# Performance work log

Measured on AMD Instinct MI355X. Metric: run time of the kernel, lower is better.

## Reference

```python
import jax, jax.numpy as jnp
import numpy as np

RES = (512, 512)
MAX_VAL = 100.0
OBJ_WIDTH = 5
N_ITERS = 5
SIGMA = 0.2


def setup_inputs() -> dict:
    key = jax.random.key(0)
    ks = jax.random.split(key, 6)
    H, W = RES
    x = jax.random.uniform(ks[0], (1, H, W, 2), jnp.float32) * 2.0 - 1.0  # query grid in [-1,1]
    boundary_types = jax.random.randint(ks[1], (H, W), 0, 2, jnp.int32)
    boundary_conditions = jax.random.uniform(ks[2], (H, W), jnp.float32)
    B_enc = SIGMA * jax.random.normal(ks[3], (64, 2), jnp.float32)  # GaussianEncoding(0.2, 2, 64)
    Wh = jax.random.normal(ks[4], (4, 128, 128), jnp.float32) / jnp.sqrt(128.0)
    W_out = jax.random.normal(ks[5], (128, 1), jnp.float32) / jnp.sqrt(128.0)
    return {"x": x, "boundary_types": boundary_types,
            "boundary_conditions": boundary_conditions,
            "B_enc": B_enc, "Wh": Wh, "W_out": W_out}


def _box_filter(a, width):
    # width x width mean filter, 'same' padding (F.conv2d with ones/width^2 kernel)
    k = jnp.ones((1, 1, width, width), a.dtype) / float(width * width)
    return jax.lax.conv_general_dilated(a[None, None], k, (1, 1), "SAME")[0, 0]


def _grid_sample_2d(img, grid):
    # img [H,W]; grid [N,2] with (x,y) in [-1,1]; bilinear, align_corners=True, border padding
    H, W = img.shape
    ix = jnp.clip((grid[:, 0] + 1.0) * 0.5 * (W - 1), 0.0, W - 1.0)
    iy = jnp.clip((grid[:, 1] + 1.0) * 0.5 * (H - 1), 0.0, H - 1.0)
    x0 = jnp.floor(ix).astype(jnp.int32)
    y0 = jnp.floor(iy).astype(jnp.int32)
    x1 = jnp.clip(x0 + 1, 0, W - 1)
    y1 = jnp.clip(y0 + 1, 0, H - 1)
    wx = ix - x0
    wy = iy - y0
    return (img[y0, x0] * (1 - wx) * (1 - wy) + img[y0, x1] * wx * (1 - wy)
            + img[y1, x0] * (1 - wx) * wy + img[y1, x1] * wx * wy)


def _solve(V0, C, boundary_types, boundary_conditions):
    # 5 Jacobi-style 8-neighbor stencil passes: free cells take the neighbor
    # average plus local cost; boundary cells are pinned to their conditions.
    free = boundary_types == 0

    def step(V, _):
        Vp = jnp.pad(V, 1, mode="edge")
        nb = (Vp[:-2, :-2] + Vp[:-2, 1:-1] + Vp[:-2, 2:]
              + Vp[1:-1, :-2] + Vp[1:-1, 2:]
              + Vp[2:, :-2] + Vp[2:, 1:-1] + Vp[2:, 2:]) / 8.0
        return jnp.where(free, nb + C, boundary_conditions), None

    V, _ = jax.lax.scan(step, V0, None, length=N_ITERS)
    return V


def reference(x, boundary_types, boundary_conditions, B_enc, Wh, W_out):
    H, W = RES
    free = boundary_types == 0
    # V init: max_val everywhere, boundary cells pinned (obj_inds = boundary_types > 0)
    V0 = jnp.where(free, jnp.float32(MAX_VAL), boundary_conditions)

    # Gaussian random Fourier feature encoding of 0.5 + 0.5*x -> 128 dims
    xq = 0.5 + 0.5 * x.reshape(-1, 2)
    vp = (2.0 * jnp.pi) * (xq @ B_enc.T)            # [N, 64]
    enc = jnp.concatenate([jnp.cos(vp), jnp.sin(vp)], axis=-1)  # [N, 128]

    # FullyFusedMLP: 4 hidden ReLU layers of 128 neurons, linear 1-dim output, no bias
    h = enc
    for i in range(Wh.shape[0]):
        h = jax.nn.relu(h @ Wh[i])
    C = (h @ W_out).reshape(H, W)
    C_pos = jax.nn.relu(C)

    # extra cost: box-filtered obstacle boundary values splashed onto free cells
    obj = boundary_conditions * (boundary_types == 1) * (boundary_conditions > 0)
    extra = _box_filter(obj, OBJ_WIDTH) * free
    Cs = C_pos + extra

    out_grid = _solve(V0, Cs, boundary_types, boundary_conditions)
    out = _grid_sample_2d(out_grid, x.reshape(-1, 2)).reshape(H, W)
    return out, C
```

## Files before the change

### kernel.cpp

```cpp
#include <hip/hip_runtime.h>
#include <hip/hip_bf16.h>


typedef unsigned short ushort_t;
typedef short short8 __attribute__((ext_vector_type(8)));
typedef float floatx16 __attribute__((ext_vector_type(16)));
typedef unsigned int uintx4 __attribute__((ext_vector_type(4)));

#define HH 512
#define WW 512
#define NPIX (HH*WW)

__device__ inline unsigned int pk_bf16(float a, float b) {
    __hip_bfloat162 h = __float22bfloat162_rn(float2{a, b});
    return *(unsigned int*)&h;
}
__device__ inline void async_copy16(void* lds, const void* g) {
    __builtin_amdgcn_global_load_lds(
        (const __attribute__((address_space(1))) unsigned int*)g,
        (__attribute__((address_space(3))) unsigned int*)lds, 16, 0, 0);
}

__global__ __launch_bounds__(256) void prep_kernel(const float* __restrict__ Wh,
                                                   ushort_t* __restrict__ WT) {
    __shared__ float trans[32][129];
    const int t = threadIdx.x;
    const int l = blockIdx.x >> 2, n0 = (blockIdx.x & 3) * 32;
    const int nl = t & 31, k0 = t >> 5;
    #pragma unroll
    for (int pass = 0; pass < 16; ++pass) {
        int k = pass * 8 + k0;
        trans[nl][k] = Wh[l * 16384 + k * 128 + n0 + nl];
    }
    __syncthreads();
    #pragma unroll
    for (int c = 0; c < 2; ++c) {
        int idx = c * 256 + t;
        int nl2 = idx >> 4, P = idx & 15;
        int n = n0 + nl2;
        int cc = P ^ (n & 15);
        int ks = cc >> 1, Hq = cc & 1;
        int base = (ks >> 1) * 32 + (ks & 1) * 16 + Hq * 4;
        unsigned int w0 = pk_bf16(trans[nl2][base + 0],  trans[nl2][base + 1]);
        unsigned int w1 = pk_bf16(trans[nl2][base + 2],  trans[nl2][base + 3]);
        unsigned int w2 = pk_bf16(trans[nl2][base + 8],  trans[nl2][base + 9]);
        unsigned int w3 = pk_bf16(trans[nl2][base + 10], trans[nl2][base + 11]);
        ((uint4*)WT)[(l * 128 + n) * 16 + P] = uint4{w0, w1, w2, w3};
    }
}

template<int BUF>
__device__ __forceinline__ void klayer(const ushort_t* __restrict__ wlds,
                                       const int (&inn)[8],
                                       const uintx4 (&fragv)[8],
                                       floatx16 (&acc)[4]) {
    #pragma unroll
    for (int i = 0; i < 4; ++i) acc[i] = (floatx16)(0.0f);
    #pragma unroll
    for (int ks = 0; ks < 8; ++ks) {
        short8 bf = __builtin_bit_cast(short8, fragv[ks]);
        #pragma unroll
        for (int i = 0; i < 4; ++i) {
            short8 av = *(const short8*)((const char*)wlds + BUF * 32768 + i * 8192 + inn[ks]);
            acc[i] = __builtin_amdgcn_mfma_f32_32x32x16_bf16(av, bf, acc[i], 0, 0, 0);
        }
    }
}

__device__ __forceinline__ void xform_all(uintx4 (&fragv)[8], const floatx16 (&acc)[4]) {
    #pragma unroll
    for (int ks = 0; ks < 8; ++ks) {
        const int i = ks >> 1, par = ks & 1;
        fragv[ks][0] = pk_bf16(fmaxf(acc[i][8 * par + 0], 0.0f),
                               fmaxf(acc[i][8 * par + 1], 0.0f));
        fragv[ks][1] = pk_bf16(fmaxf(acc[i][8 * par + 2], 0.0f),
                               fmaxf(acc[i][8 * par + 3], 0.0f));
        fragv[ks][2] = pk_bf16(fmaxf(acc[i][8 * par + 4], 0.0f),
                               fmaxf(acc[i][8 * par + 5], 0.0f));
        fragv[ks][3] = pk_bf16(fmaxf(acc[i][8 * par + 6], 0.0f),
                               fmaxf(acc[i][8 * par + 7], 0.0f));
    }
}

__device__ __forceinline__ void stage_layer(ushort_t* wlds, int buf,
                                            const char* src, int wave, int lane) {
    #pragma unroll
    for (int c2 = 0; c2 < 4; ++c2) {
        int base = c2 * 512 + wave * 64;
        async_copy16(&wlds[buf * 16384 + base * 8], src + (base + lane) * 16);
    }
}

__global__ __launch_bounds__(512, 2) void mlp_kernel(const float* __restrict__ x,
                                                     const ushort_t* __restrict__ WT,
                                                     const float* __restrict__ benc,
                                                     const float* __restrict__ wout,
                                                     float* __restrict__ C_ws,
                                                     float* __restrict__ outbuf) {
    __shared__ __align__(16) ushort_t wlds[2 * 128 * 128];
    const int tid = threadIdx.x;
    const int lane = tid & 63, wave = tid >> 6;
    const int m = lane & 31, Hh = lane >> 5;
    const int p0 = blockIdx.x * 256 + wave * 32;

    stage_layer(wlds, 0, (const char*)WT, wave, lane);
    stage_layer(wlds, 1, (const char*)WT + 32768, wave, lane);

    int inn[8];
    #pragma unroll
    for (int ks = 0; ks < 8; ++ks)
        inn[ks] = m * 256 + ((((2 * ks + Hh) ^ (m & 15))) << 4);

    uintx4 fragv[8];

    {
        float2 xv = ((const float2*)x)[p0 + m];
        float xq0 = 0.5f + 0.5f * xv.x, xq1 = 0.5f + 0.5f * xv.y;
        #pragma unroll
        for (int ks = 0; ks < 8; ++ks) {
            const int i = ks >> 1, par = ks & 1;
            #pragma unroll
            for (int jp = 0; jp < 4; ++jp) {
                int nu = i * 32 + par * 16 + Hh * 4 + (jp & 1) * 2 + (jp >> 1) * 8;
                int f = nu & 63;
                float4 b = *(const float4*)&benc[2 * f];
                float t0 = __builtin_amdgcn_fractf(xq0 * b.x + xq1 * b.y);
                float t1 = __builtin_amdgcn_fractf(xq0 * b.z + xq1 * b.w);
                float v0, v1;
                if (ks < 4) { v0 = __builtin_amdgcn_cosf(t0); v1 = __builtin_amdgcn_cosf(t1); }
                else        { v0 = __builtin_amdgcn_sinf(t0); v1 = __builtin_amdgcn_sinf(t1); }
                fragv[ks][jp] = pk_bf16(v0, v1);
            }
        }
    }
    __syncthreads();

    floatx16 acc[4];
    klayer<0>(wlds, inn, fragv, acc);
    __syncthreads();
    stage_layer(wlds, 0, (const char*)WT + 2 * 32768, wave, lane);
    xform_all(fragv, acc);
    klayer<1>(wlds, inn, fragv, acc);
    __syncthreads();
    stage_layer(wlds, 1, (const char*)WT + 3 * 32768, wave, lane);
    xform_all(fragv, acc);
    klayer<0>(wlds, inn, fragv, acc);
    __syncthreads();
    xform_all(fragv, acc);
    klayer<1>(wlds, inn, fragv, acc);

    float s = 0.0f;
    #pragma unroll
    for (int i = 0; i < 4; ++i) {
        #pragma unroll
        for (int rq = 0; rq < 4; ++rq) {
            float4 wv = *(const float4*)&wout[i * 32 + rq * 8 + 4 * Hh];
            s += fmaxf(acc[i][rq * 4 + 0], 0.0f) * wv.x
               + fmaxf(acc[i][rq * 4 + 1], 0.0f) * wv.y
               + fmaxf(acc[i][rq * 4 + 2], 0.0f) * wv.z
               + fmaxf(acc[i][rq * 4 + 3], 0.0f) * wv.w;
        }
    }
    s += __shfl_xor(s, 32);
    if (Hh == 0) {
        C_ws[p0 + m] = s;
        outbuf[NPIX + p0 + m] = s;
    }
}

__global__ __launch_bounds__(256) void fused_solve_kernel(const int* __restrict__ bt,
                                                          const float* __restrict__ bc,
                                                          const float* __restrict__ C_ws,
                                                          float* __restrict__ Vfin) {
    __shared__ float Va[30 * 32];
    __shared__ float Vb[30 * 32];
    __shared__ float Wp[30 * 32];
    const int tid = threadIdx.x;
    const int gx0 = (blockIdx.x & 31) * 16 - 7, gy0 = (blockIdx.x >> 5) * 16 - 7;

    for (int c = tid; c < 30 * 32; c += 256) {
        int li = c >> 5, lj = c & 31;
        int gi = gy0 + li, gj = gx0 + lj;
        float v = 0.0f;
        if (lj < 30 && gi >= 0 && gi < HH && gj >= 0 && gj < WW) {
            int g = gi * WW + gj;
            float b = bc[g];
            if (bt[g] == 1 && b > 0.0f) v = b;
        }
        Va[c] = v;
    }
    __syncthreads();

    for (int c = tid; c < 30 * 32; c += 256) {
        int li = c >> 5, lj = c & 31;
        int gi = gy0 + li, gj = gx0 + lj;
        float w = -1.0f, v0 = 0.0f;
        if (li >= 2 && li < 28 && lj >= 2 && lj < 28 &&
            gi >= 0 && gi < HH && gj >= 0 && gj < WW) {
            int g = gi * WW + gj;
            if (bt[g] == 0) {
                float s = 0.0f;
                #pragma unroll
                for (int di = 0; di < 5; ++di)
                    #pragma unroll
                    for (int dj = 0; dj < 5; ++dj)
                        s += Va[(li + di - 2) * 32 + lj + dj - 2];
                w = fmaxf(C_ws[g], 0.0f) + s * 0.04f;
                v0 = 100.0f;
            } else {
                float b = bc[g];
                w = -b - 1.0f;
                v0 = b;
            }
        }
        Wp[c] = w;
        Vb[c] = v0;
    }
    __syncthreads();

    float* src = Vb;
    float* dst = Va;
    #pragma unroll 1
    for (int t = 0; t < 5; ++t) {
        for (int c = tid; c < 26 * 32; c += 256) {
            int li = 2 + (c >> 5), lj = c & 31;
            if (lj < 2 || lj >= 28) continue;
            float w = Wp[li * 32 + lj];
            float v;
            if (w < 0.0f) {
                v = -w - 1.0f;
            } else {
                int gi = gy0 + li, gj = gx0 + lj;
                int um = (gi > 0)      ? li - 1 : li;
                int dp = (gi < HH - 1) ? li + 1 : li;
                int lm = (gj > 0)      ? lj - 1 : lj;
                int rp = (gj < WW - 1) ? lj + 1 : lj;
                float s = src[um * 32 + lm] + src[um * 32 + lj] + src[um * 32 + rp]
                        + src[li * 32 + lm]                     + src[li * 32 + rp]
                        + src[dp * 32 + lm] + src[dp * 32 + lj] + src[dp * 32 + rp];
                v = s * 0.125f + w;
            }
            dst[li * 32 + lj] = v;
        }
        __syncthreads();
        float* tmp = src; src = dst; dst = tmp;
    }

    {
        int li = 7 + (tid >> 4), lj = 7 + (tid & 15);
        Vfin[(gy0 + li) * WW + gx0 + lj] = src[li * 32 + lj];
    }
}

__global__ void sample_kernel(const float* __restrict__ x,
                              const float* __restrict__ V,
                              float* __restrict__ out) {
    int idx = blockIdx.x * 256 + threadIdx.x;
    float2 g2 = ((const float2*)x)[idx];
    float ix = (g2.x + 1.0f) * 0.5f * 511.0f;
    float iy = (g2.y + 1.0f) * 0.5f * 511.0f;
    ix = fminf(fmaxf(ix, 0.0f), 511.0f);
    iy = fminf(fmaxf(iy, 0.0f), 511.0f);
    int x0 = (int)floorf(ix), y0 = (int)floorf(iy);
    int x1 = min(x0 + 1, 511), y1 = min(y0 + 1, 511);
    float wx = ix - (float)x0, wy = iy - (float)y0;
    float v00 = V[y0 * 512 + x0], v01 = V[y0 * 512 + x1];
    float v10 = V[y1 * 512 + x0], v11 = V[y1 * 512 + x1];
    float v = v00 * (1.0f - wx) * (1.0f - wy) + v01 * wx * (1.0f - wy)
            + v10 * (1.0f - wx) * wy          + v11 * wx * wy;
    out[idx] = v;
}

extern "C" void kernel_launch(void* const* d_in, const int* in_sizes, int n_in,
                              void* d_out, int out_size, void* d_ws, size_t ws_size,
                              hipStream_t stream) {
    const float* x    = (const float*)d_in[0];
    const int*   bt   = (const int*)d_in[1];
    const float* bc   = (const float*)d_in[2];
    const float* benc = (const float*)d_in[3];
    const float* Wh   = (const float*)d_in[4];
    const float* wout = (const float*)d_in[5];

    char* ws = (char*)d_ws;
    ushort_t* WT   = (ushort_t*)(ws + 4096);
    float*    C_ws = (float*)(ws + 262144);
    float*    Vfin = (float*)(ws + 262144 + 3 * (1 << 20));
    float*    outp = (float*)d_out;

    prep_kernel<<<16, 256, 0, stream>>>(Wh, WT);
    mlp_kernel<<<1024, 512, 0, stream>>>(x, WT, benc, wout, C_ws, outp);
    fused_solve_kernel<<<1024, 256, 0, stream>>>(bt, bc, C_ws, Vfin);
    sample_kernel<<<1024, 256, 0, stream>>>(x, Vfin, outp);
}
```

Baseline: 118.9 us.

## Process two 32-pixel tiles per wave in MLP to reuse LDS weight fragments

Each wave in the MLP kernel now handles 64 pixels as two 32-pixel groups. Each weight fragment read from LDS feeds two MFMAs instead of one, which halves the number of blocks and the weight staging traffic per pixel. The cost is doubled accumulator and fragment registers (8 floatx16 plus 16 uintx4). With launch_bounds(512,2) that register pressure could cause spills or lower occupancy.

```diff
diff --git a/kernel.cpp b/kernel.cpp
--- a/kernel.cpp
+++ b/kernel.cpp
@@ -50,35 +50,40 @@
 }
 
 template<int BUF>
-__device__ __forceinline__ void klayer(const ushort_t* __restrict__ wlds,
-                                       const int (&inn)[8],
-                                       const uintx4 (&fragv)[8],
-                                       floatx16 (&acc)[4]) {
-    #pragma unroll
-    for (int i = 0; i < 4; ++i) acc[i] = (floatx16)(0.0f);
+__device__ __forceinline__ void klayer2(const ushort_t* __restrict__ wlds,
+                                        const int (&inn)[8],
+                                        const uintx4 (&fragv)[16],
+                                        floatx16 (&acc)[8]) {
+    #pragma unroll
+    for (int i = 0; i < 8; ++i) acc[i] = (floatx16)(0.0f);
     #pragma unroll
     for (int ks = 0; ks < 8; ++ks) {
-        short8 bf = __builtin_bit_cast(short8, fragv[ks]);
+        short8 bfA = __builtin_bit_cast(short8, fragv[ks]);
+        short8 bfB = __builtin_bit_cast(short8, fragv[8 + ks]);
         #pragma unroll
         for (int i = 0; i < 4; ++i) {
             short8 av = *(const short8*)((const char*)wlds + BUF * 32768 + i * 8192 + inn[ks]);
-            acc[i] = __builtin_amdgcn_mfma_f32_32x32x16_bf16(av, bf, acc[i], 0, 0, 0);
-        }
-    }
-}
-
-__device__ __forceinline__ void xform_all(uintx4 (&fragv)[8], const floatx16 (&acc)[4]) {
-    #pragma unroll
-    for (int ks = 0; ks < 8; ++ks) {
-        const int i = ks >> 1, par = ks & 1;
-        fragv[ks][0] = pk_bf16(fmaxf(acc[i][8 * par + 0], 0.0f),
-                               fmaxf(acc[i][8 * par + 1], 0.0f));
-        fragv[ks][1] = pk_bf16(fmaxf(acc[i][8 * par + 2], 0.0f),
-                               fmaxf(acc[i][8 * par + 3], 0.0f));
-        fragv[ks][2] = pk_bf16(fmaxf(acc[i][8 * par + 4], 0.0f),
-                               fmaxf(acc[i][8 * par + 5], 0.0f));
-        fragv[ks][3] = pk_bf16(fmaxf(acc[i][8 * par + 6], 0.0f),
-                               fmaxf(acc[i][8 * par + 7], 0.0f));
+            acc[i]     = __builtin_amdgcn_mfma_f32_32x32x16_bf16(av, bfA, acc[i],     0, 0, 0);
+            acc[4 + i] = __builtin_amdgcn_mfma_f32_32x32x16_bf16(av, bfB, acc[4 + i], 0, 0, 0);
+        }
+    }
+}
+
+__device__ __forceinline__ void xform_all2(uintx4 (&fragv)[16], const floatx16 (&acc)[8]) {
+    #pragma unroll
+    for (int g = 0; g < 2; ++g) {
+        #pragma unroll
+        for (int ks = 0; ks < 8; ++ks) {
+            const int i = (ks >> 1) + g * 4, par = ks & 1;
+            fragv[g * 8 + ks][0] = pk_bf16(fmaxf(acc[i][8 * par + 0], 0.0f),
+                                           fmaxf(acc[i][8 * par + 1], 0.0f));
+            fragv[g * 8 + ks][1] = pk_bf16(fmaxf(acc[i][8 * par + 2], 0.0f),
+                                           fmaxf(acc[i][8 * par + 3], 0.0f));
+            fragv[g * 8 + ks][2] = pk_bf16(fmaxf(acc[i][8 * par + 4], 0.0f),
+                                           fmaxf(acc[i][8 * par + 5], 0.0f));
+            fragv[g * 8 + ks][3] = pk_bf16(fmaxf(acc[i][8 * par + 6], 0.0f),
+                                           fmaxf(acc[i][8 * par + 7], 0.0f));
+        }
     }
 }
 
@@ -101,7 +106,7 @@
     const int tid = threadIdx.x;
     const int lane = tid & 63, wave = tid >> 6;
     const int m = lane & 31, Hh = lane >> 5;
-    const int p0 = blockIdx.x * 256 + wave * 32;
+    const int p0 = blockIdx.x * 512 + wave * 64;
 
     stage_layer(wlds, 0, (const char*)WT, wave, lane);
     stage_layer(wlds, 1, (const char*)WT + 32768, wave, lane);
@@ -111,10 +116,11 @@
     for (int ks = 0; ks < 8; ++ks)
         inn[ks] = m * 256 + ((((2 * ks + Hh) ^ (m & 15))) << 4);
 
-    uintx4 fragv[8];
-
-    {
-        float2 xv = ((const float2*)x)[p0 + m];
+    uintx4 fragv[16];
+
+    #pragma unroll
+    for (int g = 0; g < 2; ++g) {
+        float2 xv = ((const float2*)x)[p0 + g * 32 + m];
         float xq0 = 0.5f + 0.5f * xv.x, xq1 = 0.5f + 0.5f * xv.y;
         #pragma unroll
         for (int ks = 0; ks < 8; ++ks) {
@@ -129,42 +135,45 @@
                 float v0, v1;
                 if (ks < 4) { v0 = __builtin_amdgcn_cosf(t0); v1 = __builtin_amdgcn_cosf(t1); }
                 else        { v0 = __builtin_amdgcn_sinf(t0); v1 = __builtin_amdgcn_sinf(t1); }
-                fragv[ks][jp] = pk_bf16(v0, v1);
+                fragv[g * 8 + ks][jp] = pk_bf16(v0, v1);
             }
         }
     }
     __syncthreads();
 
-    floatx16 acc[4];
-    klayer<0>(wlds, inn, fragv, acc);
+    floatx16 acc[8];
+    klayer2<0>(wlds, inn, fragv, acc);
     __syncthreads();
     stage_layer(wlds, 0, (const char*)WT + 2 * 32768, wave, lane);
-    xform_all(fragv, acc);
-    klayer<1>(wlds, inn, fragv, acc);
+    xform_all2(fragv, acc);
+    klayer2<1>(wlds, inn, fragv, acc);
     __syncthreads();
     stage_layer(wlds, 1, (const char*)WT + 3 * 32768, wave, lane);
-    xform_all(fragv, acc);
-    klayer<0>(wlds, inn, fragv, acc);
-    __syncthreads();
-    xform_all(fragv, acc);
-    klayer<1>(wlds, inn, fragv, acc);
-
-    float s = 0.0f;
-    #pragma unroll
-    for (int i = 0; i < 4; ++i) {
+    xform_all2(fragv, acc);
+    klayer2<0>(wlds, inn, fragv, acc);
+    __syncthreads();
+    xform_all2(fragv, acc);
+    klayer2<1>(wlds, inn, fragv, acc);
+
+    #pragma unroll
+    for (int g = 0; g < 2; ++g) {
+        float s = 0.0f;
         #pragma unroll
-        for (int rq = 0; rq < 4; ++rq) {
-            float4 wv = *(const float4*)&wout[i * 32 + rq * 8 + 4 * Hh];
-            s += fmaxf(acc[i][rq * 4 + 0], 0.0f) * wv.x
-               + fmaxf(acc[i][rq * 4 + 1], 0.0f) * wv.y
-               + fmaxf(acc[i][rq * 4 + 2], 0.0f) * wv.z
-               + fmaxf(acc[i][rq * 4 + 3], 0.0f) * wv.w;
-        }
-    }
-    s += __shfl_xor(s, 32);
-    if (Hh == 0) {
-        C_ws[p0 + m] = s;
-        outbuf[NPIX + p0 + m] = s;
+        for (int i = 0; i < 4; ++i) {
+            #pragma unroll
+            for (int rq = 0; rq < 4; ++rq) {
+                float4 wv = *(const float4*)&wout[i * 32 + rq * 8 + 4 * Hh];
+                s += fmaxf(acc[g * 4 + i][rq * 4 + 0], 0.0f) * wv.x
+                   + fmaxf(acc[g * 4 + i][rq * 4 + 1], 0.0f) * wv.y
+                   + fmaxf(acc[g * 4 + i][rq * 4 + 2], 0.0f) * wv.z
+                   + fmaxf(acc[g * 4 + i][rq * 4 + 3], 0.0f) * wv.w;
+            }
+        }
+        s += __shfl_xor(s, 32);
+        if (Hh == 0) {
+            C_ws[p0 + g * 32 + m] = s;
+            outbuf[NPIX + p0 + g * 32 + m] = s;
+        }
     }
 }
 
@@ -288,7 +297,7 @@
     float*    outp = (float*)d_out;
 
     prep_kernel<<<16, 256, 0, stream>>>(Wh, WT);
-    mlp_kernel<<<1024, 512, 0, stream>>>(x, WT, benc, wout, C_ws, outp);
+    mlp_kernel<<<512, 512, 0, stream>>>(x, WT, benc, wout, C_ws, outp);
     fused_solve_kernel<<<1024, 256, 0, stream>>>(bt, bc, C_ws, Vfin);
     sample_kernel<<<1024, 256, 0, stream>>>(x, Vfin, outp);
 }
```

Measured after the change: 121.3 us. 2.0% more time.

## Enlarge solve tiles to 32x32 and make box filter separable

Applied to the files above, without the earlier changes.

The fused stencil solve now uses 32x32 output tiles with a 46x48 halo region instead of 16x16 tiles, with 256 blocks of 512 threads. This cuts the fraction of redundant halo recomputation and reloading. The 5x5 box filter becomes two separable 5-tap passes through shared memory, at the cost of one extra barrier. Fewer blocks (256) may underfill the GPU's compute units, and the index math now uses non-power-of-two divisions.

```diff
diff --git a/kernel.cpp b/kernel.cpp
--- a/kernel.cpp
+++ b/kernel.cpp
@@ -168,21 +168,25 @@
     }
 }
 
-__global__ __launch_bounds__(256) void fused_solve_kernel(const int* __restrict__ bt,
+#define LW 48
+#define LROWS 46
+#define LCELLS (LROWS * LW)
+
+__global__ __launch_bounds__(512) void fused_solve_kernel(const int* __restrict__ bt,
                                                           const float* __restrict__ bc,
                                                           const float* __restrict__ C_ws,
                                                           float* __restrict__ Vfin) {
-    __shared__ float Va[30 * 32];
-    __shared__ float Vb[30 * 32];
-    __shared__ float Wp[30 * 32];
+    __shared__ float Va[LCELLS];
+    __shared__ float Vb[LCELLS];
+    __shared__ float Wp[LCELLS];
     const int tid = threadIdx.x;
-    const int gx0 = (blockIdx.x & 31) * 16 - 7, gy0 = (blockIdx.x >> 5) * 16 - 7;
-
-    for (int c = tid; c < 30 * 32; c += 256) {
-        int li = c >> 5, lj = c & 31;
+    const int gx0 = (blockIdx.x & 15) * 32 - 7, gy0 = (blockIdx.x >> 4) * 32 - 7;
+
+    for (int c = tid; c < LCELLS; c += 512) {
+        int li = c / LW, lj = c % LW;
         int gi = gy0 + li, gj = gx0 + lj;
         float v = 0.0f;
-        if (lj < 30 && gi >= 0 && gi < HH && gj >= 0 && gj < WW) {
+        if (lj < LROWS && gi >= 0 && gi < HH && gj >= 0 && gj < WW) {
             int g = gi * WW + gj;
             float b = bc[g];
             if (bt[g] == 1 && b > 0.0f) v = b;
@@ -191,64 +195,71 @@
     }
     __syncthreads();
 
-    for (int c = tid; c < 30 * 32; c += 256) {
-        int li = c >> 5, lj = c & 31;
-        int gi = gy0 + li, gj = gx0 + lj;
+    for (int c = tid; c < LCELLS; c += 512) {
+        int lj = c % LW;
+        float s = 0.0f;
+        if (lj >= 2 && lj < LROWS - 2) {
+            s = Va[c - 2] + Va[c - 1] + Va[c] + Va[c + 1] + Va[c + 2];
+        }
+        Vb[c] = s;
+    }
+    __syncthreads();
+
+    for (int c = tid; c < LCELLS; c += 512) {
+        int li = c / LW, lj = c % LW;
         float w = -1.0f, v0 = 0.0f;
-        if (li >= 2 && li < 28 && lj >= 2 && lj < 28 &&
-            gi >= 0 && gi < HH && gj >= 0 && gj < WW) {
-            int g = gi * WW + gj;
-            if (bt[g] == 0) {
-                float s = 0.0f;
-                #pragma unroll
-                for (int di = 0; di < 5; ++di)
-                    #pragma unroll
-                    for (int dj = 0; dj < 5; ++dj)
-                        s += Va[(li + di - 2) * 32 + lj + dj - 2];
-                w = fmaxf(C_ws[g], 0.0f) + s * 0.04f;
-                v0 = 100.0f;
-            } else {
-                float b = bc[g];
-                w = -b - 1.0f;
-                v0 = b;
+        if (li >= 2 && li < LROWS - 2 && lj >= 2 && lj < LROWS - 2) {
+            int gi = gy0 + li, gj = gx0 + lj;
+            if (gi >= 0 && gi < HH && gj >= 0 && gj < WW) {
+                int g = gi * WW + gj;
+                if (bt[g] == 0) {
+                    float s = Vb[c - 2 * LW] + Vb[c - LW] + Vb[c]
+                            + Vb[c + LW] + Vb[c + 2 * LW];
+                    w = fmaxf(C_ws[g], 0.0f) + s * 0.04f;
+                    v0 = 100.0f;
+                } else {
+                    float b = bc[g];
+                    w = -b - 1.0f;
+                    v0 = b;
+                }
             }
         }
         Wp[c] = w;
-        Vb[c] = v0;
-    }
-    __syncthreads();
-
-    float* src = Vb;
-    float* dst = Va;
+        Va[c] = v0;
+    }
+    __syncthreads();
+
+    float* src = Va;
+    float* dst = Vb;
     #pragma unroll 1
     for (int t = 0; t < 5; ++t) {
-        for (int c = tid; c < 26 * 32; c += 256) {
-            int li = 2 + (c >> 5), lj = c & 31;
-            if (lj < 2 || lj >= 28) continue;
-            float w = Wp[li * 32 + lj];
+        for (int c = tid; c < LCELLS; c += 512) {
+            int li = c / LW, lj = c % LW;
+            if (li < 2 || li >= LROWS - 2 || lj < 2 || lj >= LROWS - 2) continue;
+            float w = Wp[c];
             float v;
             if (w < 0.0f) {
                 v = -w - 1.0f;
             } else {
                 int gi = gy0 + li, gj = gx0 + lj;
-                int um = (gi > 0)      ? li - 1 : li;
-                int dp = (gi < HH - 1) ? li + 1 : li;
-                int lm = (gj > 0)      ? lj - 1 : lj;
-                int rp = (gj < WW - 1) ? lj + 1 : lj;
-                float s = src[um * 32 + lm] + src[um * 32 + lj] + src[um * 32 + rp]
-                        + src[li * 32 + lm]                     + src[li * 32 + rp]
-                        + src[dp * 32 + lm] + src[dp * 32 + lj] + src[dp * 32 + rp];
+                int um = (gi > 0)      ? -LW : 0;
+                int dp = (gi < HH - 1) ?  LW : 0;
+                int lm = (gj > 0)      ?  -1 : 0;
+                int rp = (gj < WW - 1) ?   1 : 0;
+                float s = src[c + um + lm] + src[c + um] + src[c + um + rp]
+                        + src[c + lm]                     + src[c + rp]
+                        + src[c + dp + lm] + src[c + dp] + src[c + dp + rp];
                 v = s * 0.125f + w;
             }
-            dst[li * 32 + lj] = v;
+            dst[c] = v;
         }
         __syncthreads();
         float* tmp = src; src = dst; dst = tmp;
     }
 
-    {
-        int li = 7 + (tid >> 4), lj = 7 + (tid & 15);
-        Vfin[(gy0 + li) * WW + gx0 + lj] = src[li * 32 + lj];
+    for (int c = tid; c < 32 * 32; c += 512) {
+        int li = 7 + (c >> 5), lj = 7 + (c & 31);
+        Vfin[(gy0 + li) * WW + gx0 + lj] = src[li * LW + lj];
     }
 }
 
@@ -289,6 +300,6 @@
 
     prep_kernel<<<16, 256, 0, stream>>>(Wh, WT);
     mlp_kernel<<<1024, 512, 0, stream>>>(x, WT, benc, wout, C_ws, outp);
-    fused_solve_kernel<<<1024, 256, 0, stream>>>(bt, bc, C_ws, Vfin);
+    fused_solve_kernel<<<256, 512, 0, stream>>>(bt, bc, C_ws, Vfin);
     sample_kernel<<<1024, 256, 0, stream>>>(x, Vfin, outp);
 }
```

Result: no change. 119.7 us (+0.6%).
